# Kernel optimization log

Hardware: AMD Instinct MI355X
Metric: run time of the kernel (lower is better)

The kernel has to match this reference:

```python
import jax, jax.numpy as jnp
import numpy as np

B, CIN, HIN, WIN = 8192, 16, 6, 6
FM = 64                      # feature_maps
DK = FM // 2                 # 32
DV = FM // 2                 # 32
NH = FM // 2                 # 32 heads -> dkh = dvh = 1
OUT_CH = 5
HID = 128


def _conv2d(x, w, b, stride=1):
    # x: NCHW, w: OIHW, VALID padding (padding=(k-1)//2 = 0 for k=2)
    y = jax.lax.conv_general_dilated(
        x, w, window_strides=(stride, stride), padding='VALID',
        dimension_numbers=('NCHW', 'OIHW', 'NCHW'))
    return y + b[None, :, None, None]


def setup_inputs() -> dict:
    key = jax.random.key(0)
    ks = jax.random.split(key, 13)
    s = 0.1  # small init scale keeps softmax logits well-conditioned
    return {
        'x':      jax.random.normal(ks[0], (B, CIN, HIN, WIN), jnp.float32),
        # AugmentedConv: conv_out (out_channels - dv), qkv conv (2dk+dv), attn 1x1
        'conv_w': jax.random.normal(ks[1], (FM - DV, CIN, 2, 2), jnp.float32) * s,
        'conv_b': jax.random.normal(ks[2], (FM - DV,), jnp.float32) * s,
        'qkv_w':  jax.random.normal(ks[3], (2 * DK + DV, CIN, 2, 2), jnp.float32) * s,
        'qkv_b':  jax.random.normal(ks[4], (2 * DK + DV,), jnp.float32) * s,
        'attn_w': jax.random.normal(ks[5], (DV, DV, 1, 1), jnp.float32) * s,
        'attn_b': jax.random.normal(ks[6], (DV,), jnp.float32) * s,
        # DoubleDense: fm*5*5 -> hid -> hid//2 -> out
        'w1': jax.random.normal(ks[7], (HID, FM * 5 * 5), jnp.float32) * s,
        'b1': jax.random.normal(ks[8], (HID,), jnp.float32) * s,
        'w2': jax.random.normal(ks[9], (HID // 2, HID), jnp.float32) * s,
        'b2': jax.random.normal(ks[10], (HID // 2,), jnp.float32) * s,
        'w3': jax.random.normal(ks[11], (OUT_CH, HID // 2), jnp.float32) * s,
        'b3': jax.random.normal(ks[12], (OUT_CH,), jnp.float32) * s,
    }


def _forward(x, conv_w, conv_b, qkv_w, qkv_b, attn_w, attn_b, w1, b1, w2, b2, w3, b3):
    # ---- AugmentedConv ----
    conv_out = _conv2d(x, conv_w, conv_b)            # [B, FM-DV, 5, 5]
    qkv = _conv2d(x, qkv_w, qkv_b)                   # [B, 2DK+DV, 5, 5]
    b, _, h, w = qkv.shape
    q, k, v = jnp.split(qkv, [DK, 2 * DK], axis=1)
    dkh = DK // NH
    q = q * (dkh ** -0.5)
    flat_q = q.reshape(b, NH, dkh, h * w)            # [B, Nh, dkh, HW]
    flat_k = k.reshape(b, NH, dkh, h * w)
    flat_v = v.reshape(b, NH, DV // NH, h * w)
    # logits = q^T k over head-dim: [B, Nh, HW, HW]
    logits = jnp.einsum('bndi,bndj->bnij', flat_q, flat_k)
    weights = jax.nn.softmax(logits, axis=-1)
    # attn = weights @ v^T -> [B, Nh, HW, dvh]
    attn = jnp.einsum('bnij,bnjd->bnid', weights, flat_v.transpose(0, 1, 3, 2))
    # faithful to torch: raw reshape (B, Nh, dvh, H, W) then combine heads
    attn = attn.reshape(b, NH, DV // NH, h, w).reshape(b, DV, h, w)
    attn = _conv2d(attn, attn_w, attn_b)             # 1x1 conv
    y = jnp.concatenate([conv_out, attn], axis=1)    # [B, FM, 5, 5]
    # ---- ReLU + DoubleDense ----
    y = jax.nn.relu(y).reshape(b, -1)                # [B, FM*25]
    y = jax.nn.relu(y @ w1.T + b1)
    y = jax.nn.relu(y @ w2.T + b2)
    return y @ w3.T + b3                             # [B, OUT_CH]


def reference(x, conv_w, conv_b, qkv_w, qkv_b, attn_w, attn_b, w1, b1, w2, b2, w3, b3):
    return _forward(x, conv_w, conv_b, qkv_w, qkv_b, attn_w, attn_b,
                    w1, b1, w2, b2, w3, b3)
```

## Files before the change

kernel.cpp:

```cpp
#include <hip/hip_runtime.h>
#include <hip/hip_bf16.h>
#include <cstdint>
#include <cstddef>


typedef __attribute__((ext_vector_type(4))) float f32x4;
typedef __attribute__((ext_vector_type(2))) float f32x2;
typedef __attribute__((ext_vector_type(8))) __bf16 bf16x8;
typedef __attribute__((ext_vector_type(4))) __bf16 bf16x4;

#define LOG2E 1.4426950408889634f

__device__ __forceinline__ float fast_exp2(float x) {
#if __has_builtin(__builtin_amdgcn_exp2f)
  return __builtin_amdgcn_exp2f(x);
#else
  return __expf(x * 0.6931471805599453f);
#endif
}

__device__ __forceinline__ f32x4 mfma16(bf16x8 a, bf16x8 b, f32x4 c) {
  return __builtin_amdgcn_mfma_f32_16x16x32_bf16(a, b, c, 0, 0, 0);
}

__global__ __launch_bounds__(64) void prep_small(
    const float* __restrict__ conv_w, const float* __restrict__ conv_b,
    const float* __restrict__ qkv_w,  const float* __restrict__ qkv_b,
    const float* __restrict__ attn_w,
    __hip_bfloat16* __restrict__ wqb, float* __restrict__ biasb,
    __hip_bfloat16* __restrict__ wab) {
  const int t = threadIdx.x, tb = blockIdx.x;
  if (tb < 16) {
#pragma unroll
    for (int j = 0; j < 8; ++j) {
      int i = tb * 512 + j * 64 + t;
      float w = (i < 2048) ? conv_w[i] : qkv_w[i - 2048];
      if (i >= 4096 && i < 6144) w *= LOG2E;
      wqb[i] = __float2bfloat16(w);
    }
  } else {
#pragma unroll
    for (int j = 0; j < 16; ++j) wab[j * 64 + t] = __float2bfloat16(attn_w[j * 64 + t]);
    for (int i = t; i < 128; i += 64) {
      float b = (i < 32) ? conv_b[i] : qkv_b[i - 32];
      if (i >= 64 && i < 96) b *= LOG2E;
      biasb[i] = b;
    }
  }
}

__global__ __launch_bounds__(128) void k1(
    const float* __restrict__ x,
    const float* __restrict__ biasb,
    const __hip_bfloat16* __restrict__ wqb,
    const __hip_bfloat16* __restrict__ wab, const float* __restrict__ attn_b,
    const float* __restrict__ w1, const float* __restrict__ w2,
    __hip_bfloat16* __restrict__ act,
    __hip_bfloat16* __restrict__ w1bp, __hip_bfloat16* __restrict__ w2b) {
  const int t = threadIdx.x & 63;
  const int wv = threadIdx.x >> 6;

  __shared__ __align__(16) char lds_raw[2 * 7168];
  char* my = lds_raw + wv * 7168;

  if (blockIdx.x >= 4096) {
    const int u = (blockIdx.x - 4096) * 2 + wv;
    if (u < 128) {
      float* rowf = (float*)my;
      const float* wr = w1 + u * 1600;
#pragma unroll
      for (int j = 0; j < 25; ++j) rowf[j * 64 + t] = wr[j * 64 + t];
      __hip_bfloat16* wo = w1bp + u * 1600;
#pragma unroll
      for (int j = 0; j < 25; ++j) {
        wo[j * 64 + t] = __float2bfloat16(rowf[t * 25 + j]);
      }
    } else if (u < 132) {
#pragma unroll
      for (int j = 0; j < 32; ++j) {
        int i = (u - 128) * 2048 + j * 64 + t;
        w2b[i] = __float2bfloat16(w2[i]);
      }
    }
    return;
  }

  const int l15 = t & 15, quad = t >> 4;
  const int b = blockIdx.x * 2 + wv;
  __bf16* xs  = (__bf16*)my;
  __bf16* as_ = (__bf16*)my;
  __bf16* qs  = (__bf16*)(my + 1600);

  const float* xb = x + (size_t)b * 576;
#pragma unroll
  for (int i = 0; i < 9; ++i) {
    int f = t + i * 64;
    xs[f] = __float2bfloat16(xb[f]);
  }

  bf16x8 bfr[8][2];
#pragma unroll
  for (int nt = 0; nt < 8; ++nt)
#pragma unroll
    for (int ks = 0; ks < 2; ++ks)
      bfr[nt][ks] = *(const bf16x8*)((const __bf16*)wqb + (nt * 16 + l15) * 64 + ks * 32 + quad * 8);
  float bias[8];
#pragma unroll
  for (int nt = 0; nt < 8; ++nt) bias[nt] = biasb[nt * 16 + l15];

#pragma unroll
  for (int mt = 0; mt < 2; ++mt) {
    int row = mt * 16 + l15;
    int pos = row < 24 ? row : 24;
    int ii = pos / 5, jj = pos - ii * 5;
    const __bf16* xp = xs + ii * 6 + jj;
    bf16x8 af[2];
#pragma unroll
    for (int ks = 0; ks < 2; ++ks) {
      const __bf16* p0 = xp + (ks * 8 + quad * 2) * 36;
      bf16x8 a;
      a[0] = p0[0];  a[1] = p0[1];  a[2] = p0[6];  a[3] = p0[7];
      a[4] = p0[36]; a[5] = p0[37]; a[6] = p0[42]; a[7] = p0[43];
      af[ks] = a;
    }
    f32x4 acc[8];
#pragma unroll
    for (int nt = 0; nt < 8; ++nt) acc[nt] = (f32x4){0.f, 0.f, 0.f, 0.f};
#pragma unroll
    for (int ks = 0; ks < 2; ++ks)
#pragma unroll
      for (int nt = 0; nt < 8; ++nt)
        acc[nt] = mfma16(af[ks], bfr[nt][ks], acc[nt]);

#pragma unroll
    for (int r = 0; r < 4; ++r) {
      int orow = mt * 16 + quad * 4 + r;
      if (orow < 25) {
#pragma unroll
        for (int nt = 0; nt < 8; ++nt) {
          float v = acc[nt][r] + bias[nt];
          if (nt < 2) {
            act[((size_t)b * 25 + orow) * 64 + nt * 16 + l15] =
                __float2bfloat16(fmaxf(v, 0.f));
          } else {
            qs[((nt - 2) * 16 + l15) * 28 + orow] = __float2bfloat16(v);
          }
        }
      }
    }
  }

  {
    const int n = t & 31, half = t >> 5;
    const __bf16* qp = qs + n * 28;
    const __bf16* kp = qs + (32 + n) * 28;
    const __bf16* vp = qs + (64 + n) * 28;
    f32x2 kl2[12], vv2[12];
    float kl24, vv24;
#pragma unroll
    for (int c4 = 0; c4 < 6; ++c4) {
      bf16x4 bb = *(const bf16x4*)(kp + c4 * 4);
      bf16x4 cc = *(const bf16x4*)(vp + c4 * 4);
      kl2[c4 * 2]     = (f32x2){(float)bb[0], (float)bb[1]};
      kl2[c4 * 2 + 1] = (f32x2){(float)bb[2], (float)bb[3]};
      vv2[c4 * 2]     = (f32x2){(float)cc[0], (float)cc[1]};
      vv2[c4 * 2 + 1] = (f32x2){(float)cc[2], (float)cc[3]};
    }
    kl24 = (float)kp[24]; vv24 = (float)vp[24];

    const int i0 = half * 12;
    float qv[13];
    {
      const __bf16* qbase = qp + i0;
      bf16x4 q0 = *(const bf16x4*)(qbase);
      bf16x4 q1 = *(const bf16x4*)(qbase + 4);
      bf16x4 q2 = *(const bf16x4*)(qbase + 8);
#pragma unroll
      for (int z = 0; z < 4; ++z) {
        qv[z] = (float)q0[z]; qv[4 + z] = (float)q1[z]; qv[8 + z] = (float)q2[z];
      }
      qv[12] = (float)qbase[12];
    }

#pragma unroll
    for (int z = 0; z < 13; ++z) {
      const float qi = qv[z];
      const f32x2 qi2 = {qi, qi};
      f32x2 sA = {0.f, 0.f}, sB = {0.f, 0.f};
      f32x2 oA = {0.f, 0.f}, oB = {0.f, 0.f};
      float s4 = 0.f, o4 = 0.f;
#pragma unroll
      for (int p = 0; p < 6; ++p) {
        f32x2 mA = qi2 * kl2[p];
        f32x2 mB = qi2 * kl2[p + 6];
        f32x2 eA = {fast_exp2(mA.x), fast_exp2(mA.y)};
        f32x2 eB = {fast_exp2(mB.x), fast_exp2(mB.y)};
        sA += eA;
        sB += eB;
        oA = eA * vv2[p] + oA;
        oB = eB * vv2[p + 6] + oB;
      }
      {
        float e = fast_exp2(qi * kl24);
        s4 += e;
        o4 = __builtin_fmaf(e, vv24, o4);
      }
      float ss = ((sA.x + sA.y) + (sB.x + sB.y)) + s4;
      float oo = ((oA.x + oA.y) + (oB.x + oB.y)) + o4;
      as_[(i0 + z) * 32 + n] = __float2bfloat16(oo * __builtin_amdgcn_rcpf(ss));
    }
  }

  {
    bf16x8 bw[2]; float ab[2];
#pragma unroll
    for (int nt2 = 0; nt2 < 2; ++nt2) {
      int n = nt2 * 16 + l15;
      bw[nt2] = *(const bf16x8*)((const __bf16*)wab + n * 32 + quad * 8);
      ab[nt2] = attn_b[n];
    }
#pragma unroll
    for (int mt = 0; mt < 2; ++mt) {
      int row = mt * 16 + l15;
      int rc = row < 24 ? row : 24;
      bf16x8 af = *(const bf16x8*)(as_ + rc * 32 + quad * 8);
      f32x4 acc[2];
#pragma unroll
      for (int nt2 = 0; nt2 < 2; ++nt2)
        acc[nt2] = mfma16(af, bw[nt2], (f32x4){0.f, 0.f, 0.f, 0.f});
#pragma unroll
      for (int r = 0; r < 4; ++r) {
        int orow = mt * 16 + quad * 4 + r;
        if (orow < 25) {
#pragma unroll
          for (int nt2 = 0; nt2 < 2; ++nt2)
            act[((size_t)b * 25 + orow) * 64 + 32 + nt2 * 16 + l15] =
                __float2bfloat16(fmaxf(acc[nt2][r] + ab[nt2], 0.f));
        }
      }
    }
  }
}

__global__ __launch_bounds__(512) void k2(
    const __hip_bfloat16* __restrict__ act,
    const __hip_bfloat16* __restrict__ w1bp, const float* __restrict__ b1,
    const __hip_bfloat16* __restrict__ w2b, const float* __restrict__ b2,
    const float* __restrict__ w3, const float* __restrict__ b3,
    float* __restrict__ out) {
  const int t = threadIdx.x;
  const int lane = t & 63;
  const int wave = t >> 6;
  const int wm = wave >> 2;
  const int wn = wave & 3;
  const int l15 = lane & 15;
  const int quad = lane >> 4;
  const int b0 = blockIdx.x * 32;

  __shared__ __hip_bfloat16 C1s[32 * 136];
  __shared__ __hip_bfloat16 C2s[32 * 72];

  f32x4 acc0 = {0.f, 0.f, 0.f, 0.f};
  f32x4 acc1 = {0.f, 0.f, 0.f, 0.f};
  const __bf16* aptr  = (const __bf16*)act + (size_t)(b0 + wm * 16 + l15) * 1600 + quad * 8;
  const __bf16* bptr0 = (const __bf16*)w1bp + (size_t)(wn * 32 + l15) * 1600 + quad * 8;
  const __bf16* bptr1 = bptr0 + 16 * 1600;
#pragma unroll 5
  for (int k0 = 0; k0 < 1600; k0 += 32) {
    bf16x8 av  = *(const bf16x8*)(aptr + k0);
    bf16x8 bv0 = *(const bf16x8*)(bptr0 + k0);
    bf16x8 bv1 = *(const bf16x8*)(bptr1 + k0);
    acc0 = mfma16(av, bv0, acc0);
    acc1 = mfma16(av, bv1, acc1);
  }
  {
    const int col0 = wn * 32 + l15;
    const float bias0 = b1[col0];
    const float bias1 = b1[col0 + 16];
#pragma unroll
    for (int r = 0; r < 4; ++r) {
      const int row = wm * 16 + quad * 4 + r;
      C1s[row * 136 + col0]      = __float2bfloat16(fmaxf(acc0[r] + bias0, 0.f));
      C1s[row * 136 + col0 + 16] = __float2bfloat16(fmaxf(acc1[r] + bias1, 0.f));
    }
  }
  __syncthreads();

  f32x4 acc2 = {0.f, 0.f, 0.f, 0.f};
  {
    const __bf16* aL = (const __bf16*)C1s + (wm * 16 + l15) * 136 + quad * 8;
    const __bf16* bL = (const __bf16*)w2b + (wn * 16 + l15) * 128 + quad * 8;
#pragma unroll
    for (int k0 = 0; k0 < 128; k0 += 32)
      acc2 = mfma16(*(const bf16x8*)(aL + k0), *(const bf16x8*)(bL + k0), acc2);
  }
  {
    const int col = wn * 16 + l15;
    const float bias = b2[col];
#pragma unroll
    for (int r = 0; r < 4; ++r) {
      const int row = wm * 16 + quad * 4 + r;
      C2s[row * 72 + col] = __float2bfloat16(fmaxf(acc2[r] + bias, 0.f));
    }
  }
  __syncthreads();

  if (t < 160) {
    const int row = t / 5;
    const int oc = t - row * 5;
    float s = b3[oc];
#pragma unroll
    for (int k = 0; k < 64; ++k)
      s += __bfloat162float(C2s[row * 72 + k]) * w3[oc * 64 + k];
    out[(size_t)(b0 + row) * 5 + oc] = s;
  }
}

extern "C" void kernel_launch(void* const* d_in, const int* in_sizes, int n_in,
                              void* d_out, int out_size, void* d_ws, size_t ws_size,
                              hipStream_t stream) {
  const float* x      = (const float*)d_in[0];
  const float* conv_w = (const float*)d_in[1];
  const float* conv_b = (const float*)d_in[2];
  const float* qkv_w  = (const float*)d_in[3];
  const float* qkv_b  = (const float*)d_in[4];
  const float* attn_w = (const float*)d_in[5];
  const float* attn_b = (const float*)d_in[6];
  const float* w1 = (const float*)d_in[7];
  const float* b1 = (const float*)d_in[8];
  const float* w2 = (const float*)d_in[9];
  const float* b2 = (const float*)d_in[10];
  const float* w3 = (const float*)d_in[11];
  const float* b3 = (const float*)d_in[12];
  float* out = (float*)d_out;

  char* ws = (char*)d_ws;
  __hip_bfloat16* act   = (__hip_bfloat16*)ws;
  __hip_bfloat16* w1bp  = (__hip_bfloat16*)(ws + 26214400);
  __hip_bfloat16* w2b   = (__hip_bfloat16*)(ws + 26624000);
  __hip_bfloat16* wqb   = (__hip_bfloat16*)(ws + 26640384);
  float*          biasb = (float*)(ws + 26656768);
  __hip_bfloat16* wab   = (__hip_bfloat16*)(ws + 26657280);

  prep_small<<<dim3(17), dim3(64), 0, stream>>>(conv_w, conv_b, qkv_w, qkv_b, attn_w,
                                                wqb, biasb, wab);
  k1<<<dim3(4096 + 66), dim3(128), 0, stream>>>(x, biasb, wqb, wab, attn_b,
                                                w1, w2, act, w1bp, w2b);
  k2<<<dim3(256), dim3(512), 0, stream>>>(act, w1bp, b1, w2b, b2, w3, b3, out);
}
```

Measured before the change: 158.6 us.

## Process two samples per wave in k1 and prefetch second input during attention

Each wave in k1 now handles two batch samples instead of one, which halves the grid. Per-wave weight fragments (qkv, bias, attn 1x1) are loaded once and reused for both samples. The second sample's input is loaded from global memory into registers while the first sample's softmax-attention phase runs, then staged into a separate LDS region. This amortises the weight loads and hides global load latency, but raises register and LDS use per wave (8 KB per wave) and may lower occupancy.

```diff
diff --git a/kernel.cpp b/kernel.cpp
--- a/kernel.cpp
+++ b/kernel.cpp
@@ -45,6 +45,146 @@
       float b = (i < 32) ? conv_b[i] : qkv_b[i - 32];
       if (i >= 64 && i < 96) b *= LOG2E;
       biasb[i] = b;
+    }
+  }
+}
+
+
+struct WaveCtx {
+  int t, l15, quad;
+  bf16x8 bfr[8][2];
+  float bias[8];
+  bf16x8 bw[2];
+  float ab[2];
+};
+
+__device__ __forceinline__ void phase1(
+    const WaveCtx& c, int b, const __bf16* xs, __bf16* qs,
+    __hip_bfloat16* __restrict__ act) {
+#pragma unroll
+  for (int mt = 0; mt < 2; ++mt) {
+    int row = mt * 16 + c.l15;
+    int pos = row < 24 ? row : 24;
+    int ii = pos / 5, jj = pos - ii * 5;
+    const __bf16* xp = xs + ii * 6 + jj;
+    bf16x8 af[2];
+#pragma unroll
+    for (int ks = 0; ks < 2; ++ks) {
+      const __bf16* p0 = xp + (ks * 8 + c.quad * 2) * 36;
+      bf16x8 a;
+      a[0] = p0[0];  a[1] = p0[1];  a[2] = p0[6];  a[3] = p0[7];
+      a[4] = p0[36]; a[5] = p0[37]; a[6] = p0[42]; a[7] = p0[43];
+      af[ks] = a;
+    }
+    f32x4 acc[8];
+#pragma unroll
+    for (int nt = 0; nt < 8; ++nt) acc[nt] = (f32x4){0.f, 0.f, 0.f, 0.f};
+#pragma unroll
+    for (int ks = 0; ks < 2; ++ks)
+#pragma unroll
+      for (int nt = 0; nt < 8; ++nt)
+        acc[nt] = mfma16(af[ks], c.bfr[nt][ks], acc[nt]);
+
+#pragma unroll
+    for (int r = 0; r < 4; ++r) {
+      int orow = mt * 16 + c.quad * 4 + r;
+      if (orow < 25) {
+#pragma unroll
+        for (int nt = 0; nt < 8; ++nt) {
+          float v = acc[nt][r] + c.bias[nt];
+          if (nt < 2) {
+            act[((size_t)b * 25 + orow) * 64 + nt * 16 + c.l15] =
+                __float2bfloat16(fmaxf(v, 0.f));
+          } else {
+            qs[((nt - 2) * 16 + c.l15) * 28 + orow] = __float2bfloat16(v);
+          }
+        }
+      }
+    }
+  }
+}
+
+__device__ __forceinline__ void phase2(const WaveCtx& c, const __bf16* qs, __bf16* as_) {
+  const int n = c.t & 31, half = c.t >> 5;
+  const __bf16* qp = qs + n * 28;
+  const __bf16* kp = qs + (32 + n) * 28;
+  const __bf16* vp = qs + (64 + n) * 28;
+  f32x2 kl2[12], vv2[12];
+  float kl24, vv24;
+#pragma unroll
+  for (int c4 = 0; c4 < 6; ++c4) {
+    bf16x4 bb = *(const bf16x4*)(kp + c4 * 4);
+    bf16x4 cc = *(const bf16x4*)(vp + c4 * 4);
+    kl2[c4 * 2]     = (f32x2){(float)bb[0], (float)bb[1]};
+    kl2[c4 * 2 + 1] = (f32x2){(float)bb[2], (float)bb[3]};
+    vv2[c4 * 2]     = (f32x2){(float)cc[0], (float)cc[1]};
+    vv2[c4 * 2 + 1] = (f32x2){(float)cc[2], (float)cc[3]};
+  }
+  kl24 = (float)kp[24]; vv24 = (float)vp[24];
+
+  const int i0 = half * 12;
+  float qv[13];
+  {
+    const __bf16* qbase = qp + i0;
+    bf16x4 q0 = *(const bf16x4*)(qbase);
+    bf16x4 q1 = *(const bf16x4*)(qbase + 4);
+    bf16x4 q2 = *(const bf16x4*)(qbase + 8);
+#pragma unroll
+    for (int z = 0; z < 4; ++z) {
+      qv[z] = (float)q0[z]; qv[4 + z] = (float)q1[z]; qv[8 + z] = (float)q2[z];
+    }
+    qv[12] = (float)qbase[12];
+  }
+
+#pragma unroll
+  for (int z = 0; z < 13; ++z) {
+    const float qi = qv[z];
+    const f32x2 qi2 = {qi, qi};
+    f32x2 sA = {0.f, 0.f}, sB = {0.f, 0.f};
+    f32x2 oA = {0.f, 0.f}, oB = {0.f, 0.f};
+    float s4 = 0.f, o4 = 0.f;
+#pragma unroll
+    for (int p = 0; p < 6; ++p) {
+      f32x2 mA = qi2 * kl2[p];
+      f32x2 mB = qi2 * kl2[p + 6];
+      f32x2 eA = {fast_exp2(mA.x), fast_exp2(mA.y)};
+      f32x2 eB = {fast_exp2(mB.x), fast_exp2(mB.y)};
+      sA += eA;
+      sB += eB;
+      oA = eA * vv2[p] + oA;
+      oB = eB * vv2[p + 6] + oB;
+    }
+    {
+      float e = fast_exp2(qi * kl24);
+      s4 += e;
+      o4 = __builtin_fmaf(e, vv24, o4);
+    }
+    float ss = ((sA.x + sA.y) + (sB.x + sB.y)) + s4;
+    float oo = ((oA.x + oA.y) + (oB.x + oB.y)) + o4;
+    as_[(i0 + z) * 32 + n] = __float2bfloat16(oo * __builtin_amdgcn_rcpf(ss));
+  }
+}
+
+__device__ __forceinline__ void phase3(
+    const WaveCtx& c, int b, const __bf16* as_, __hip_bfloat16* __restrict__ act) {
+#pragma unroll
+  for (int mt = 0; mt < 2; ++mt) {
+    int row = mt * 16 + c.l15;
+    int rc = row < 24 ? row : 24;
+    bf16x8 af = *(const bf16x8*)(as_ + rc * 32 + c.quad * 8);
+    f32x4 acc[2];
+#pragma unroll
+    for (int nt2 = 0; nt2 < 2; ++nt2)
+      acc[nt2] = mfma16(af, c.bw[nt2], (f32x4){0.f, 0.f, 0.f, 0.f});
+#pragma unroll
+    for (int r = 0; r < 4; ++r) {
+      int orow = mt * 16 + c.quad * 4 + r;
+      if (orow < 25) {
+#pragma unroll
+        for (int nt2 = 0; nt2 < 2; ++nt2)
+          act[((size_t)b * 25 + orow) * 64 + 32 + nt2 * 16 + c.l15] =
+              __float2bfloat16(fmaxf(acc[nt2][r] + c.ab[nt2], 0.f));
+      }
     }
   }
 }
@@ -60,11 +200,11 @@
   const int t = threadIdx.x & 63;
   const int wv = threadIdx.x >> 6;
 
-  __shared__ __align__(16) char lds_raw[2 * 7168];
-  char* my = lds_raw + wv * 7168;
-
-  if (blockIdx.x >= 4096) {
-    const int u = (blockIdx.x - 4096) * 2 + wv;
+  __shared__ __align__(16) char lds_raw[2 * 8192];
+  char* my = lds_raw + wv * 8192;
+
+  if (blockIdx.x >= 2048) {
+    const int u = (blockIdx.x - 2048) * 2 + wv;
     if (u < 128) {
       float* rowf = (float*)my;
       const float* wr = w1 + u * 1600;
@@ -85,161 +225,53 @@
     return;
   }
 
-  const int l15 = t & 15, quad = t >> 4;
-  const int b = blockIdx.x * 2 + wv;
-  __bf16* xs  = (__bf16*)my;
-  __bf16* as_ = (__bf16*)my;
+  WaveCtx c;
+  c.t = t; c.l15 = t & 15; c.quad = t >> 4;
+  const int w = blockIdx.x * 2 + wv;
+  const int bA = w * 2, bB = w * 2 + 1;
+
+  __bf16* ra  = (__bf16*)my;
   __bf16* qs  = (__bf16*)(my + 1600);
-
-  const float* xb = x + (size_t)b * 576;
+  __bf16* xsB = (__bf16*)(my + 6976);
+
+  const float* xbA = x + (size_t)bA * 576;
 #pragma unroll
   for (int i = 0; i < 9; ++i) {
     int f = t + i * 64;
-    xs[f] = __float2bfloat16(xb[f]);
-  }
-
-  bf16x8 bfr[8][2];
+    ra[f] = __float2bfloat16(xbA[f]);
+  }
+
 #pragma unroll
   for (int nt = 0; nt < 8; ++nt)
 #pragma unroll
     for (int ks = 0; ks < 2; ++ks)
-      bfr[nt][ks] = *(const bf16x8*)((const __bf16*)wqb + (nt * 16 + l15) * 64 + ks * 32 + quad * 8);
-  float bias[8];
-#pragma unroll
-  for (int nt = 0; nt < 8; ++nt) bias[nt] = biasb[nt * 16 + l15];
-
-#pragma unroll
-  for (int mt = 0; mt < 2; ++mt) {
-    int row = mt * 16 + l15;
-    int pos = row < 24 ? row : 24;
-    int ii = pos / 5, jj = pos - ii * 5;
-    const __bf16* xp = xs + ii * 6 + jj;
-    bf16x8 af[2];
-#pragma unroll
-    for (int ks = 0; ks < 2; ++ks) {
-      const __bf16* p0 = xp + (ks * 8 + quad * 2) * 36;
-      bf16x8 a;
-      a[0] = p0[0];  a[1] = p0[1];  a[2] = p0[6];  a[3] = p0[7];
-      a[4] = p0[36]; a[5] = p0[37]; a[6] = p0[42]; a[7] = p0[43];
-      af[ks] = a;
-    }
-    f32x4 acc[8];
-#pragma unroll
-    for (int nt = 0; nt < 8; ++nt) acc[nt] = (f32x4){0.f, 0.f, 0.f, 0.f};
-#pragma unroll
-    for (int ks = 0; ks < 2; ++ks)
-#pragma unroll
-      for (int nt = 0; nt < 8; ++nt)
-        acc[nt] = mfma16(af[ks], bfr[nt][ks], acc[nt]);
-
-#pragma unroll
-    for (int r = 0; r < 4; ++r) {
-      int orow = mt * 16 + quad * 4 + r;
-      if (orow < 25) {
-#pragma unroll
-        for (int nt = 0; nt < 8; ++nt) {
-          float v = acc[nt][r] + bias[nt];
-          if (nt < 2) {
-            act[((size_t)b * 25 + orow) * 64 + nt * 16 + l15] =
-                __float2bfloat16(fmaxf(v, 0.f));
-          } else {
-            qs[((nt - 2) * 16 + l15) * 28 + orow] = __float2bfloat16(v);
-          }
-        }
-      }
-    }
-  }
-
-  {
-    const int n = t & 31, half = t >> 5;
-    const __bf16* qp = qs + n * 28;
-    const __bf16* kp = qs + (32 + n) * 28;
-    const __bf16* vp = qs + (64 + n) * 28;
-    f32x2 kl2[12], vv2[12];
-    float kl24, vv24;
-#pragma unroll
-    for (int c4 = 0; c4 < 6; ++c4) {
-      bf16x4 bb = *(const bf16x4*)(kp + c4 * 4);
-      bf16x4 cc = *(const bf16x4*)(vp + c4 * 4);
-      kl2[c4 * 2]     = (f32x2){(float)bb[0], (float)bb[1]};
-      kl2[c4 * 2 + 1] = (f32x2){(float)bb[2], (float)bb[3]};
-      vv2[c4 * 2]     = (f32x2){(float)cc[0], (float)cc[1]};
-      vv2[c4 * 2 + 1] = (f32x2){(float)cc[2], (float)cc[3]};
-    }
-    kl24 = (float)kp[24]; vv24 = (float)vp[24];
-
-    const int i0 = half * 12;
-    float qv[13];
-    {
-      const __bf16* qbase = qp + i0;
-      bf16x4 q0 = *(const bf16x4*)(qbase);
-      bf16x4 q1 = *(const bf16x4*)(qbase + 4);
-      bf16x4 q2 = *(const bf16x4*)(qbase + 8);
-#pragma unroll
-      for (int z = 0; z < 4; ++z) {
-        qv[z] = (float)q0[z]; qv[4 + z] = (float)q1[z]; qv[8 + z] = (float)q2[z];
-      }
-      qv[12] = (float)qbase[12];
-    }
-
-#pragma unroll
-    for (int z = 0; z < 13; ++z) {
-      const float qi = qv[z];
-      const f32x2 qi2 = {qi, qi};
-      f32x2 sA = {0.f, 0.f}, sB = {0.f, 0.f};
-      f32x2 oA = {0.f, 0.f}, oB = {0.f, 0.f};
-      float s4 = 0.f, o4 = 0.f;
-#pragma unroll
-      for (int p = 0; p < 6; ++p) {
-        f32x2 mA = qi2 * kl2[p];
-        f32x2 mB = qi2 * kl2[p + 6];
-        f32x2 eA = {fast_exp2(mA.x), fast_exp2(mA.y)};
-        f32x2 eB = {fast_exp2(mB.x), fast_exp2(mB.y)};
-        sA += eA;
-        sB += eB;
-        oA = eA * vv2[p] + oA;
-        oB = eB * vv2[p + 6] + oB;
-      }
-      {
-        float e = fast_exp2(qi * kl24);
-        s4 += e;
-        o4 = __builtin_fmaf(e, vv24, o4);
-      }
-      float ss = ((sA.x + sA.y) + (sB.x + sB.y)) + s4;
-      float oo = ((oA.x + oA.y) + (oB.x + oB.y)) + o4;
-      as_[(i0 + z) * 32 + n] = __float2bfloat16(oo * __builtin_amdgcn_rcpf(ss));
-    }
-  }
-
-  {
-    bf16x8 bw[2]; float ab[2];
-#pragma unroll
-    for (int nt2 = 0; nt2 < 2; ++nt2) {
-      int n = nt2 * 16 + l15;
-      bw[nt2] = *(const bf16x8*)((const __bf16*)wab + n * 32 + quad * 8);
-      ab[nt2] = attn_b[n];
-    }
-#pragma unroll
-    for (int mt = 0; mt < 2; ++mt) {
-      int row = mt * 16 + l15;
-      int rc = row < 24 ? row : 24;
-      bf16x8 af = *(const bf16x8*)(as_ + rc * 32 + quad * 8);
-      f32x4 acc[2];
-#pragma unroll
-      for (int nt2 = 0; nt2 < 2; ++nt2)
-        acc[nt2] = mfma16(af, bw[nt2], (f32x4){0.f, 0.f, 0.f, 0.f});
-#pragma unroll
-      for (int r = 0; r < 4; ++r) {
-        int orow = mt * 16 + quad * 4 + r;
-        if (orow < 25) {
-#pragma unroll
-          for (int nt2 = 0; nt2 < 2; ++nt2)
-            act[((size_t)b * 25 + orow) * 64 + 32 + nt2 * 16 + l15] =
-                __float2bfloat16(fmaxf(acc[nt2][r] + ab[nt2], 0.f));
-        }
-      }
-    }
-  }
+      c.bfr[nt][ks] = *(const bf16x8*)((const __bf16*)wqb + (nt * 16 + c.l15) * 64 + ks * 32 + c.quad * 8);
+#pragma unroll
+  for (int nt = 0; nt < 8; ++nt) c.bias[nt] = biasb[nt * 16 + c.l15];
+#pragma unroll
+  for (int nt2 = 0; nt2 < 2; ++nt2) {
+    int n = nt2 * 16 + c.l15;
+    c.bw[nt2] = *(const bf16x8*)((const __bf16*)wab + n * 32 + c.quad * 8);
+    c.ab[nt2] = attn_b[n];
+  }
+
+  phase1(c, bA, ra, qs, act);
+
+  float xf[9];
+  const float* xbB = x + (size_t)bB * 576;
+#pragma unroll
+  for (int i = 0; i < 9; ++i) xf[i] = xbB[t + i * 64];
+
+  phase2(c, qs, ra);
+
+#pragma unroll
+  for (int i = 0; i < 9; ++i) xsB[t + i * 64] = __float2bfloat16(xf[i]);
+
+  phase3(c, bA, ra, act);
+
+  phase1(c, bB, xsB, qs, act);
+  phase2(c, qs, ra);
+  phase3(c, bB, ra, act);
 }
 
 __global__ __launch_bounds__(512) void k2(
@@ -344,7 +376,7 @@
 
   prep_small<<<dim3(17), dim3(64), 0, stream>>>(conv_w, conv_b, qkv_w, qkv_b, attn_w,
                                                 wqb, biasb, wab);
-  k1<<<dim3(4096 + 66), dim3(128), 0, stream>>>(x, biasb, wqb, wab, attn_b,
+  k1<<<dim3(2048 + 66), dim3(128), 0, stream>>>(x, biasb, wqb, wab, attn_b,
                                                 w1, w2, act, w1bp, w2b);
   k2<<<dim3(256), dim3(512), 0, stream>>>(act, w1bp, b1, w2b, b2, w3, b3, out);
 }
```

After: 166.0 us. 4.6% more time.
